# Kernel optimization log

Hardware: AMD Instinct MI355X
Metric: run time of the kernel (lower is better)

The kernel has to match this reference:

```python
import jax, jax.numpy as jnp
import numpy as np

B, S, E, H = 2, 2048, 1024, 16
DH = E // H


def setup_inputs() -> dict:
    key = jax.random.key(0)
    ks = jax.random.split(key, 9)
    inp = {
        "query": jax.random.normal(ks[0], (B, S, E), dtype=jnp.float32),
        "key": jax.random.normal(ks[1], (B, S, E), dtype=jnp.float32),
        "value": jax.random.normal(ks[2], (B, S, E), dtype=jnp.float32),
        # causal mask: True means "masked out" (masked_fill semantics)
        "mask": jnp.broadcast_to(
            jnp.triu(jnp.ones((S, S), dtype=bool), k=1)[None, None], (B, 1, S, S)
        ),
        # learned parameters (nn.Linear weight is [out, in]; y = x @ W.T + b)
        "Wq": jax.random.normal(ks[3], (E, E), dtype=jnp.float32) / np.sqrt(E),
        "Wk": jax.random.normal(ks[4], (E, E), dtype=jnp.float32) / np.sqrt(E),
        "Wv": jax.random.normal(ks[5], (E, E), dtype=jnp.float32) / np.sqrt(E),
        "Wo": jax.random.normal(ks[6], (E, E), dtype=jnp.float32) / np.sqrt(E),
        "bo": jax.random.normal(ks[7], (E,), dtype=jnp.float32) * 0.01,
    }
    return inp


def reference(query, key, value, mask, Wq, Wk, Wv, Wo, bo):
    # projections (no bias for q/k/v)
    Q = query @ Wq.T  # [B,S,E]
    K = key @ Wk.T
    V = value @ Wv.T
    # split heads: [B,S,E] -> [B,H,S,Dh]
    Q = Q.reshape(B, S, H, DH).transpose(0, 2, 1, 3)
    K = K.reshape(B, S, H, DH).transpose(0, 2, 1, 3)
    V = V.reshape(B, S, H, DH).transpose(0, 2, 1, 3)
    scale = 1.0 / np.sqrt(DH).astype(np.float32)
    scores = jnp.einsum("bhqd,bhkd->bhqk", Q, K) * scale  # [B,H,S,S]
    scores = jnp.where(mask, -jnp.inf, scores)
    attn = jax.nn.softmax(scores, axis=-1)
    # dropout(p=0.2) is identity in eval mode
    out = jnp.einsum("bhqk,bhkd->bhqd", attn, V)  # [B,H,S,Dh]
    out = out.transpose(0, 2, 1, 3).reshape(B, S, E)
    return out @ Wo.T + bo
```

## Files before the change

### kernel.cpp

```cpp
#include <hip/hip_runtime.h>
#include <hip/hip_bf16.h>
#include <stdint.h>

#define Bb 2
#define Ss 2048
#define Ee 1024
#define Hh 16
#define Dh 64

typedef __bf16 bf16_t;
typedef __attribute__((ext_vector_type(8))) __bf16 bf16x8;
typedef __attribute__((ext_vector_type(4))) __bf16 bf16x4;
typedef __attribute__((ext_vector_type(4))) float f32x4;

#define QSCALE_LOG2E 0.18033688011112042f

__device__ inline void gload_lds16(const void* g, void* l) {
  __builtin_amdgcn_global_load_lds((__attribute__((address_space(1))) void*)g,
                                   (__attribute__((address_space(3))) void*)l,
                                   16, 0, 0);
}

__device__ inline void wg_barrier() {
  asm volatile("s_barrier" ::: "memory");
}

__device__ __forceinline__ int p_addr(int q, int kv) {
  return q * 256 + ((((kv >> 3) ^ q) & 15) << 4) + (kv & 7) * 2;
}

struct Cvt7 {
  const float* s[7];
  bf16_t* d[7];
  int n8[7];
};

__global__ __launch_bounds__(256) void cvt_f32_bf16(Cvt7 c) {
  int gid = blockIdx.x * 256 + threadIdx.x;
#pragma unroll
  for (int j = 0; j < 7; ++j) {
    if (gid < c.n8[j]) {
      const float* s = c.s[j] + (size_t)gid * 8;
      const f32x4 lo = *(const f32x4*)s;
      const f32x4 hi = *(const f32x4*)(s + 4);
      bf16x8 v;
      v[0] = (bf16_t)lo[0]; v[1] = (bf16_t)lo[1];
      v[2] = (bf16_t)lo[2]; v[3] = (bf16_t)lo[3];
      v[4] = (bf16_t)hi[0]; v[5] = (bf16_t)hi[1];
      v[6] = (bf16_t)hi[2]; v[7] = (bf16_t)hi[3];
      *(bf16x8*)(c.d[j] + (size_t)gid * 8) = v;
      return;
    }
    gid -= c.n8[j];
  }
}

template <int ROWS>
__device__ __forceinline__ void stage_bf16(const bf16_t* __restrict__ src,
                                           int ldk, int k0, bf16_t* lds,
                                           int wave, int lane) {
  const int srow = lane >> 3, sslot = lane & 7;
#pragma unroll
  for (int r = 0; r < ROWS / 32; ++r) {
    const int chunk = wave + r * 4;
    const int row = chunk * 8 + srow;
    const int k16 = sslot ^ (row & 7);
    gload_lds16(src + (size_t)row * ldk + k0 + k16 * 8, lds + chunk * 512);
  }
}

template <typename EPI>
__device__ __forceinline__ void gemm_128x64(const bf16_t* Arow,
                                            const bf16_t* Wrow, bf16_t* As,
                                            bf16_t* Bs, int wave, int lane,
                                            EPI epi) {
  const int lr = lane & 15, lg = lane >> 4;
  f32x4 acc[2][4] = {};

  stage_bf16<128>(Arow, Ee, 0, As, wave, lane);
  stage_bf16<64>(Wrow, Ee, 0, Bs, wave, lane);
  stage_bf16<128>(Arow, Ee, 64, As + 8192, wave, lane);
  stage_bf16<64>(Wrow, Ee, 64, Bs + 4096, wave, lane);

  for (int t = 0; t < 16; ++t) {
    const int cur = t & 1;
    if (t < 15)
      asm volatile("s_waitcnt vmcnt(6)" ::: "memory");
    else
      asm volatile("s_waitcnt vmcnt(0)" ::: "memory");
    wg_barrier();

    const char* a_base = (const char*)(As + cur * 8192);
    const char* b_base = (const char*)(Bs + cur * 4096);
#pragma unroll
    for (int kk = 0; kk < 2; ++kk) {
      bf16x8 af[2], bfr[4];
#pragma unroll
      for (int x = 0; x < 2; ++x) {
        const int arow = wave * 32 + x * 16 + lr;
        af[x] = *(const bf16x8*)(a_base + ((arow * 128 + kk * 64 + lg * 16) ^
                                           ((arow & 7) << 4)));
      }
#pragma unroll
      for (int ni = 0; ni < 4; ++ni) {
        const int brow = ni * 16 + lr;
        bfr[ni] = *(const bf16x8*)(b_base + ((brow * 128 + kk * 64 + lg * 16) ^
                                             ((brow & 7) << 4)));
      }
#pragma unroll
      for (int mi = 0; mi < 2; ++mi)
#pragma unroll
        for (int ni = 0; ni < 4; ++ni)
          acc[mi][ni] = __builtin_amdgcn_mfma_f32_16x16x32_bf16(
              af[mi], bfr[ni], acc[mi][ni], 0, 0, 0);
    }
    wg_barrier();
    if (t + 2 < 16) {
      stage_bf16<128>(Arow, Ee, (t + 2) * 64, As + cur * 8192, wave, lane);
      stage_bf16<64>(Wrow, Ee, (t + 2) * 64, Bs + cur * 4096, wave, lane);
    }
  }

#pragma unroll
  for (int mi = 0; mi < 2; ++mi)
#pragma unroll
    for (int i = 0; i < 4; ++i) {
      const int mloc = wave * 32 + mi * 16 + lg * 4 + i;
#pragma unroll
      for (int ni = 0; ni < 4; ++ni)
        epi(mloc, ni * 16 + lr, acc[mi][ni][i]);
    }
}

__global__ __launch_bounds__(256) void qkv_proj(
    const bf16_t* __restrict__ Aq, const bf16_t* __restrict__ Ak,
    const bf16_t* __restrict__ Av, const bf16_t* __restrict__ Wq,
    const bf16_t* __restrict__ Wk, const bf16_t* __restrict__ Wv,
    bf16_t* __restrict__ Cq, bf16_t* __restrict__ Ck,
    bf16_t* __restrict__ Cv) {
  __shared__ bf16_t As[2][128 * 64];
  __shared__ bf16_t Bs[2][64 * 64];
  const int z = blockIdx.z;
  const bf16_t* A = (z == 0) ? Aq : (z == 1) ? Ak : Av;
  const bf16_t* W = (z == 0) ? Wq : (z == 1) ? Wk : Wv;
  bf16_t* C = (z == 0) ? Cq : (z == 1) ? Ck : Cv;

  const int wg = blockIdx.y * 16 + blockIdx.x;
  const int virt = (wg & 7) * 64 + (wg >> 3);
  const int n0 = (virt & 15) * 64, m0 = (virt >> 4) * 128;

  const int lane = threadIdx.x & 63, wave = threadIdx.x >> 6;

  gemm_128x64(A + (size_t)m0 * Ee, W + (size_t)n0 * Ee, As[0], Bs[0], wave,
              lane, [&](int mloc, int nloc, float v) {
                const int m = m0 + mloc, n = n0 + nloc;
                if (z == 0) v *= QSCALE_LOG2E;
                const int b = m >> 11, s = m & (Ss - 1);
                const int h = n >> 6, d = n & 63;
                if (z != 2)
                  C[(((size_t)(b * Hh + h)) * Ss + s) * Dh + d] = (bf16_t)v;
                else
                  C[(((size_t)(b * Hh + h)) * Dh + d) * Ss + s] = (bf16_t)v;
              });
}

__global__ __launch_bounds__(256) void out_gemm(const bf16_t* __restrict__ A,
                                                const bf16_t* __restrict__ W,
                                                const float* __restrict__ bias,
                                                float* __restrict__ C) {
  __shared__ bf16_t As[2][128 * 64];
  __shared__ bf16_t Bs[2][64 * 64];
  const int wg = blockIdx.y * 16 + blockIdx.x;
  const int virt = (wg & 7) * 64 + (wg >> 3);
  const int n0 = (virt & 15) * 64, m0 = (virt >> 4) * 128;

  const int lane = threadIdx.x & 63, wave = threadIdx.x >> 6;

  gemm_128x64(A + (size_t)m0 * Ee, W + (size_t)n0 * Ee, As[0], Bs[0], wave,
              lane, [&](int mloc, int nloc, float v) {
                const int n = n0 + nloc;
                C[(size_t)(m0 + mloc) * Ee + n] = v + bias[n];
              });
}


__device__ __forceinline__ void attn_stage(const bf16_t* Kh, const bf16_t* Vh,
                                           int kv0, int wave, int lane,
                                           bf16_t* KsBuf, bf16_t* VsBuf) {
#pragma unroll
  for (int r = 0; r < 4; ++r) {
    const int c = wave + r * 4;
    const int krow = c * 8 + (lane >> 3);
    const int ks = (lane & 7) ^ (krow & 7);
    gload_lds16(Kh + (size_t)(kv0 + krow) * Dh + ks * 8, KsBuf + c * 512);
    const int vrow = c * 4 + (lane >> 4);
    const int vs = (lane & 15) ^ (vrow & 7);
    gload_lds16(Vh + (size_t)vrow * Ss + kv0 + vs * 8, VsBuf + c * 512);
  }
}

template <int NI, bool MASKED>
__device__ __forceinline__ void attn_tile_compute(
    int kv0, int qw, int lane, char* pb, const char* kb, const char* vb,
    const bf16x8 aq[2], float& m_run, float& l_run, f32x4 oacc[4]) {
  const int lr = lane & 15, lg = lane >> 4;

  f32x4 sc[NI];
#pragma unroll
  for (int ni = 0; ni < NI; ++ni) {
    const int krow = ni * 16 + lr;
    const bf16x8 ak0 =
        *(const bf16x8*)(kb + ((krow * 128 + lg * 16) ^ ((krow & 7) << 4)));
    const bf16x8 ak1 = *(const bf16x8*)(kb + ((krow * 128 + 64 + lg * 16) ^
                                              ((krow & 7) << 4)));
    f32x4 z = {0.f, 0.f, 0.f, 0.f};
    z = __builtin_amdgcn_mfma_f32_16x16x32_bf16(ak0, aq[0], z, 0, 0, 0);
    z = __builtin_amdgcn_mfma_f32_16x16x32_bf16(ak1, aq[1], z, 0, 0, 0);
    sc[ni] = z;
  }

  if (MASKED) {
    const int q_rel = qw + lr - kv0;
#pragma unroll
    for (int ni = 0; ni < NI; ++ni)
#pragma unroll
      for (int i = 0; i < 4; ++i)
        if (ni * 16 + lg * 4 + i > q_rel) sc[ni][i] = -1e30f;
  }

  f32x4 vm = sc[0];
#pragma unroll
  for (int ni = 1; ni < NI; ++ni)
#pragma unroll
    for (int i = 0; i < 4; ++i) vm[i] = fmaxf(vm[i], sc[ni][i]);
  float rm = fmaxf(fmaxf(vm[0], vm[1]), fmaxf(vm[2], vm[3]));
  rm = fmaxf(rm, __shfl_xor(rm, 16));
  rm = fmaxf(rm, __shfl_xor(rm, 32));

  const float mo = m_run;
  const float mn = fmaxf(mo, rm);
  const float corr = __builtin_amdgcn_exp2f(mo - mn);
  m_run = mn;

  f32x4 vs = {0.f, 0.f, 0.f, 0.f};
#pragma unroll
  for (int ni = 0; ni < NI; ++ni) {
    bf16x4 w;
#pragma unroll
    for (int i = 0; i < 4; ++i) {
      const float p = __builtin_amdgcn_exp2f(sc[ni][i] - mn);
      vs[i] += p;
      w[i] = (bf16_t)p;
    }
    *(bf16x4*)(pb + p_addr(lr, ni * 16 + lg * 4)) = w;
  }
  float rs = (vs[0] + vs[1]) + (vs[2] + vs[3]);
  rs += __shfl_xor(rs, 16);
  rs += __shfl_xor(rs, 32);
  l_run = l_run * corr + rs;

#pragma unroll
  for (int i = 0; i < 4; ++i) {
    const float ci = __shfl(corr, (lane & 48) | (lg * 4 + i));
#pragma unroll
    for (int di = 0; di < 4; ++di) oacc[di][i] *= ci;
  }

#pragma unroll
  for (int kk = 0; kk < NI / 2; ++kk) {
    const bf16x8 pa = *(const bf16x8*)(pb + p_addr(lr, kk * 32 + lg * 8));
#pragma unroll
    for (int di = 0; di < 4; ++di) {
      const int vrow = di * 16 + lr;
      const bf16x8 bv = *(const bf16x8*)(vb + ((vrow * 256 + kk * 64 +
                                                lg * 16) ^
                                               ((vrow & 7) << 4)));
      oacc[di] =
          __builtin_amdgcn_mfma_f32_16x16x32_bf16(pa, bv, oacc[di], 0, 0, 0);
    }
  }
}

__device__ __forceinline__ void flash_qtile(int qt, const bf16_t* Qh,
                                            const bf16_t* Kh, const bf16_t* Vh,
                                            bf16_t* AO_row, int wave, int lane,
                                            bf16_t* Ks, bf16_t* Vs,
                                            bf16_t* PsW) {
  const int lr = lane & 15, lg = lane >> 4;
  const int qw = qt * 64 + wave * 16;

  bf16x8 aq[2];
#pragma unroll
  for (int kd = 0; kd < 2; ++kd)
    aq[kd] = *(const bf16x8*)(Qh + (size_t)(qw + lr) * Dh + kd * 32 + lg * 8);

  f32x4 oacc[4] = {};
  float m_run = -1e30f, l_run = 0.f;
  char* pb = (char*)PsW;

  const int nt = (qt + 2) >> 1;
  attn_stage(Kh, Vh, 0, wave, lane, Ks, Vs);

  for (int t = 0; t < nt; ++t) {
    const int cur = t & 1;
    if (t + 1 < nt) {
      attn_stage(Kh, Vh, (t + 1) * 128, wave, lane, Ks + (cur ^ 1) * 8192,
                 Vs + (cur ^ 1) * 8192);
      asm volatile("s_waitcnt vmcnt(8)" ::: "memory");
    } else {
      asm volatile("s_waitcnt vmcnt(0)" ::: "memory");
    }
    wg_barrier();
    const char* kb = (const char*)(Ks + cur * 8192);
    const char* vb = (const char*)(Vs + cur * 8192);
    if (t < nt - 1)
      attn_tile_compute<8, false>(t * 128, qw, lane, pb, kb, vb, aq, m_run,
                                  l_run, oacc);
    else if ((qt & 1) == 0)
      attn_tile_compute<4, true>(t * 128, qw, lane, pb, kb, vb, aq, m_run,
                                 l_run, oacc);
    else
      attn_tile_compute<8, true>(t * 128, qw, lane, pb, kb, vb, aq, m_run,
                                 l_run, oacc);
    wg_barrier();
  }

#pragma unroll
  for (int i = 0; i < 4; ++i) {
    const float li = __shfl(l_run, (lane & 48) | (lg * 4 + i));
    const float inv = 1.0f / li;
    const int s = qw + lg * 4 + i;
#pragma unroll
    for (int di = 0; di < 4; ++di) {
      const int d = di * 16 + lr;
      AO_row[(size_t)s * Ee + d] = (bf16_t)(oacc[di][i] * inv);
    }
  }
}

__global__ __launch_bounds__(256, 2) void attn_causal(
    const bf16_t* __restrict__ Qg, const bf16_t* __restrict__ Kg,
    const bf16_t* __restrict__ Vg, bf16_t* __restrict__ AO) {
  const int wg = blockIdx.y * 16 + blockIdx.x;
  const int virt = (wg & 7) * 64 + (wg >> 3);
  const int qx = virt & 15;
  const int bh = virt >> 4;

  const int tid = threadIdx.x;
  const int lane = tid & 63, wave = tid >> 6;

  const bf16_t* Qh = Qg + (size_t)bh * Ss * Dh;
  const bf16_t* Kh = Kg + (size_t)bh * Ss * Dh;
  const bf16_t* Vh = Vg + (size_t)bh * Dh * Ss;
  const int b = bh >> 4, h = bh & 15;
  bf16_t* AO_row = AO + (size_t)b * Ss * Ee + h * 64;

  __shared__ bf16_t Ks[2][128 * 64];
  __shared__ bf16_t Vs[2][64 * 128];
  __shared__ bf16_t Ps[4][16 * 128];

  const int qtA = qx;
  const int qtB = 31 - qx;
  flash_qtile(qtA, Qh, Kh, Vh, AO_row, wave, lane, Ks[0], Vs[0], Ps[wave]);
  flash_qtile(qtB, Qh, Kh, Vh, AO_row, wave, lane, Ks[0], Vs[0], Ps[wave]);
}

extern "C" void kernel_launch(void* const* d_in, const int* in_sizes, int n_in,
                              void* d_out, int out_size, void* d_ws,
                              size_t ws_size, hipStream_t stream) {
  const float* query = (const float*)d_in[0];
  const float* key = (const float*)d_in[1];
  const float* value = (const float*)d_in[2];
  const float* Wq = (const float*)d_in[4];
  const float* Wk = (const float*)d_in[5];
  const float* Wv = (const float*)d_in[6];
  const float* Wo = (const float*)d_in[7];
  const float* bo = (const float*)d_in[8];

  const size_t T = (size_t)Bb * Ss * Ee;
  const size_t WN = (size_t)Ee * Ee;
  bf16_t* qbf = (bf16_t*)d_ws;
  bf16_t* kbf = qbf + T;
  bf16_t* vbf = kbf + T;
  bf16_t* wqb = vbf + T;
  bf16_t* wkb = wqb + WN;
  bf16_t* wvb = wkb + WN;
  bf16_t* wob = wvb + WN;
  bf16_t* qws = wob + WN;
  bf16_t* kws = qws + T;
  bf16_t* vws = kws + T;
  bf16_t* aows = qbf;

  Cvt7 c;
  c.s[0] = query; c.d[0] = qbf; c.n8[0] = (int)(T / 8);
  c.s[1] = key;   c.d[1] = kbf; c.n8[1] = (int)(T / 8);
  c.s[2] = value; c.d[2] = vbf; c.n8[2] = (int)(T / 8);
  c.s[3] = Wq;    c.d[3] = wqb; c.n8[3] = (int)(WN / 8);
  c.s[4] = Wk;    c.d[4] = wkb; c.n8[4] = (int)(WN / 8);
  c.s[5] = Wv;    c.d[5] = wvb; c.n8[5] = (int)(WN / 8);
  c.s[6] = Wo;    c.d[6] = wob; c.n8[6] = (int)(WN / 8);
  const int total8 = (int)((3 * T + 4 * WN) / 8);

  dim3 blk(256);
  cvt_f32_bf16<<<dim3(total8 / 256), blk, 0, stream>>>(c);
  qkv_proj<<<dim3(Ee / 64, (Bb * Ss) / 128, 3), blk, 0, stream>>>(
      qbf, kbf, vbf, wqb, wkb, wvb, qws, kws, vws);
  attn_causal<<<dim3(16, Bb * Hh), blk, 0, stream>>>(qws, kws, vws, aows);
  out_gemm<<<dim3(Ee / 64, (Bb * Ss) / 128), blk, 0, stream>>>(
      aows, wob, bo, (float*)d_out);
}
```

Measured before the change: 113.3 us.

## Give each attention wave two 16-row query blocks with half the waves

The attention kernel now runs 2 waves of 128 threads per workgroup instead of 4, and each wave handles 32 query rows (two 16-row sub-tiles) instead of 16. Each K and V fragment read from LDS feeds two MFMAs, which halves LDS reads per unit of compute. Each wave now issues twice as many async global-to-LDS loads, so the waitcnt threshold is raised to match. The risks are higher register pressure and fewer waves per workgroup to hide latency, since the grid size is unchanged and total resident waves drop.

After: 124.1 us. +9.6%, slower.

```diff
diff --git a/kernel.cpp b/kernel.cpp
--- a/kernel.cpp
+++ b/kernel.cpp
@@ -188,8 +188,8 @@
                                            int kv0, int wave, int lane,
                                            bf16_t* KsBuf, bf16_t* VsBuf) {
 #pragma unroll
-  for (int r = 0; r < 4; ++r) {
-    const int c = wave + r * 4;
+  for (int r = 0; r < 8; ++r) {
+    const int c = wave + r * 2;
     const int krow = c * 8 + (lane >> 3);
     const int ks = (lane & 7) ^ (krow & 7);
     gload_lds16(Kh + (size_t)(kv0 + krow) * Dh + ks * 8, KsBuf + c * 512);
@@ -202,10 +202,10 @@
 template <int NI, bool MASKED>
 __device__ __forceinline__ void attn_tile_compute(
     int kv0, int qw, int lane, char* pb, const char* kb, const char* vb,
-    const bf16x8 aq[2], float& m_run, float& l_run, f32x4 oacc[4]) {
+    const bf16x8 aq[2][2], float m_run[2], float l_run[2], f32x4 oacc[2][4]) {
   const int lr = lane & 15, lg = lane >> 4;
 
-  f32x4 sc[NI];
+  f32x4 sc[2][NI];
 #pragma unroll
   for (int ni = 0; ni < NI; ++ni) {
     const int krow = ni * 16 + lr;
@@ -213,70 +213,83 @@
         *(const bf16x8*)(kb + ((krow * 128 + lg * 16) ^ ((krow & 7) << 4)));
     const bf16x8 ak1 = *(const bf16x8*)(kb + ((krow * 128 + 64 + lg * 16) ^
                                               ((krow & 7) << 4)));
-    f32x4 z = {0.f, 0.f, 0.f, 0.f};
-    z = __builtin_amdgcn_mfma_f32_16x16x32_bf16(ak0, aq[0], z, 0, 0, 0);
-    z = __builtin_amdgcn_mfma_f32_16x16x32_bf16(ak1, aq[1], z, 0, 0, 0);
-    sc[ni] = z;
-  }
-
-  if (MASKED) {
-    const int q_rel = qw + lr - kv0;
-#pragma unroll
-    for (int ni = 0; ni < NI; ++ni)
-#pragma unroll
-      for (int i = 0; i < 4; ++i)
-        if (ni * 16 + lg * 4 + i > q_rel) sc[ni][i] = -1e30f;
-  }
-
-  f32x4 vm = sc[0];
-#pragma unroll
-  for (int ni = 1; ni < NI; ++ni)
-#pragma unroll
-    for (int i = 0; i < 4; ++i) vm[i] = fmaxf(vm[i], sc[ni][i]);
-  float rm = fmaxf(fmaxf(vm[0], vm[1]), fmaxf(vm[2], vm[3]));
-  rm = fmaxf(rm, __shfl_xor(rm, 16));
-  rm = fmaxf(rm, __shfl_xor(rm, 32));
-
-  const float mo = m_run;
-  const float mn = fmaxf(mo, rm);
-  const float corr = __builtin_amdgcn_exp2f(mo - mn);
-  m_run = mn;
-
-  f32x4 vs = {0.f, 0.f, 0.f, 0.f};
-#pragma unroll
-  for (int ni = 0; ni < NI; ++ni) {
-    bf16x4 w;
+#pragma unroll
+    for (int qj = 0; qj < 2; ++qj) {
+      f32x4 z = {0.f, 0.f, 0.f, 0.f};
+      z = __builtin_amdgcn_mfma_f32_16x16x32_bf16(ak0, aq[qj][0], z, 0, 0, 0);
+      z = __builtin_amdgcn_mfma_f32_16x16x32_bf16(ak1, aq[qj][1], z, 0, 0, 0);
+      sc[qj][ni] = z;
+    }
+  }
+
+  float corr[2];
+#pragma unroll
+  for (int qj = 0; qj < 2; ++qj) {
+    if (MASKED) {
+      const int q_rel = qw + qj * 16 + lr - kv0;
+#pragma unroll
+      for (int ni = 0; ni < NI; ++ni)
+#pragma unroll
+        for (int i = 0; i < 4; ++i)
+          if (ni * 16 + lg * 4 + i > q_rel) sc[qj][ni][i] = -1e30f;
+    }
+
+    f32x4 vm = sc[qj][0];
+#pragma unroll
+    for (int ni = 1; ni < NI; ++ni)
+#pragma unroll
+      for (int i = 0; i < 4; ++i) vm[i] = fmaxf(vm[i], sc[qj][ni][i]);
+    float rm = fmaxf(fmaxf(vm[0], vm[1]), fmaxf(vm[2], vm[3]));
+    rm = fmaxf(rm, __shfl_xor(rm, 16));
+    rm = fmaxf(rm, __shfl_xor(rm, 32));
+
+    const float mo = m_run[qj];
+    const float mn = fmaxf(mo, rm);
+    corr[qj] = __builtin_amdgcn_exp2f(mo - mn);
+    m_run[qj] = mn;
+
+    f32x4 vs = {0.f, 0.f, 0.f, 0.f};
+#pragma unroll
+    for (int ni = 0; ni < NI; ++ni) {
+      bf16x4 w;
+#pragma unroll
+      for (int i = 0; i < 4; ++i) {
+        const float p = __builtin_amdgcn_exp2f(sc[qj][ni][i] - mn);
+        vs[i] += p;
+        w[i] = (bf16_t)p;
+      }
+      *(bf16x4*)(pb + p_addr(qj * 16 + lr, ni * 16 + lg * 4)) = w;
+    }
+    float rs = (vs[0] + vs[1]) + (vs[2] + vs[3]);
+    rs += __shfl_xor(rs, 16);
+    rs += __shfl_xor(rs, 32);
+    l_run[qj] = l_run[qj] * corr[qj] + rs;
+
 #pragma unroll
     for (int i = 0; i < 4; ++i) {
-      const float p = __builtin_amdgcn_exp2f(sc[ni][i] - mn);
-      vs[i] += p;
-      w[i] = (bf16_t)p;
-    }
-    *(bf16x4*)(pb + p_addr(lr, ni * 16 + lg * 4)) = w;
-  }
-  float rs = (vs[0] + vs[1]) + (vs[2] + vs[3]);
-  rs += __shfl_xor(rs, 16);
-  rs += __shfl_xor(rs, 32);
-  l_run = l_run * corr + rs;
-
-#pragma unroll
-  for (int i = 0; i < 4; ++i) {
-    const float ci = __shfl(corr, (lane & 48) | (lg * 4 + i));
-#pragma unroll
-    for (int di = 0; di < 4; ++di) oacc[di][i] *= ci;
+      const float ci = __shfl(corr[qj], (lane & 48) | (lg * 4 + i));
+#pragma unroll
+      for (int di = 0; di < 4; ++di) oacc[qj][di][i] *= ci;
+    }
   }
 
 #pragma unroll
   for (int kk = 0; kk < NI / 2; ++kk) {
-    const bf16x8 pa = *(const bf16x8*)(pb + p_addr(lr, kk * 32 + lg * 8));
+    bf16x8 pa[2];
+#pragma unroll
+    for (int qj = 0; qj < 2; ++qj)
+      pa[qj] =
+          *(const bf16x8*)(pb + p_addr(qj * 16 + lr, kk * 32 + lg * 8));
 #pragma unroll
     for (int di = 0; di < 4; ++di) {
       const int vrow = di * 16 + lr;
       const bf16x8 bv = *(const bf16x8*)(vb + ((vrow * 256 + kk * 64 +
                                                 lg * 16) ^
                                                ((vrow & 7) << 4)));
-      oacc[di] =
-          __builtin_amdgcn_mfma_f32_16x16x32_bf16(pa, bv, oacc[di], 0, 0, 0);
+#pragma unroll
+      for (int qj = 0; qj < 2; ++qj)
+        oacc[qj][di] = __builtin_amdgcn_mfma_f32_16x16x32_bf16(
+            pa[qj], bv, oacc[qj][di], 0, 0, 0);
     }
   }
 }
@@ -287,15 +300,18 @@
                                             bf16_t* Ks, bf16_t* Vs,
                                             bf16_t* PsW) {
   const int lr = lane & 15, lg = lane >> 4;
-  const int qw = qt * 64 + wave * 16;
-
-  bf16x8 aq[2];
-#pragma unroll
-  for (int kd = 0; kd < 2; ++kd)
-    aq[kd] = *(const bf16x8*)(Qh + (size_t)(qw + lr) * Dh + kd * 32 + lg * 8);
-
-  f32x4 oacc[4] = {};
-  float m_run = -1e30f, l_run = 0.f;
+  const int qw = qt * 64 + wave * 32;
+
+  bf16x8 aq[2][2];
+#pragma unroll
+  for (int qj = 0; qj < 2; ++qj)
+#pragma unroll
+    for (int kd = 0; kd < 2; ++kd)
+      aq[qj][kd] = *(const bf16x8*)(Qh + (size_t)(qw + qj * 16 + lr) * Dh +
+                                    kd * 32 + lg * 8);
+
+  f32x4 oacc[2][4] = {};
+  float m_run[2] = {-1e30f, -1e30f}, l_run[2] = {0.f, 0.f};
   char* pb = (char*)PsW;
 
   const int nt = (qt + 2) >> 1;
@@ -306,7 +322,7 @@
     if (t + 1 < nt) {
       attn_stage(Kh, Vh, (t + 1) * 128, wave, lane, Ks + (cur ^ 1) * 8192,
                  Vs + (cur ^ 1) * 8192);
-      asm volatile("s_waitcnt vmcnt(8)" ::: "memory");
+      asm volatile("s_waitcnt vmcnt(16)" ::: "memory");
     } else {
       asm volatile("s_waitcnt vmcnt(0)" ::: "memory");
     }
@@ -326,19 +342,22 @@
   }
 
 #pragma unroll
-  for (int i = 0; i < 4; ++i) {
-    const float li = __shfl(l_run, (lane & 48) | (lg * 4 + i));
-    const float inv = 1.0f / li;
-    const int s = qw + lg * 4 + i;
-#pragma unroll
-    for (int di = 0; di < 4; ++di) {
-      const int d = di * 16 + lr;
-      AO_row[(size_t)s * Ee + d] = (bf16_t)(oacc[di][i] * inv);
-    }
-  }
-}
-
-__global__ __launch_bounds__(256, 2) void attn_causal(
+  for (int qj = 0; qj < 2; ++qj) {
+#pragma unroll
+    for (int i = 0; i < 4; ++i) {
+      const float li = __shfl(l_run[qj], (lane & 48) | (lg * 4 + i));
+      const float inv = 1.0f / li;
+      const int s = qw + qj * 16 + lg * 4 + i;
+#pragma unroll
+      for (int di = 0; di < 4; ++di) {
+        const int d = di * 16 + lr;
+        AO_row[(size_t)s * Ee + d] = (bf16_t)(oacc[qj][di][i] * inv);
+      }
+    }
+  }
+}
+
+__global__ __launch_bounds__(128, 2) void attn_causal(
     const bf16_t* __restrict__ Qg, const bf16_t* __restrict__ Kg,
     const bf16_t* __restrict__ Vg, bf16_t* __restrict__ AO) {
   const int wg = blockIdx.y * 16 + blockIdx.x;
@@ -357,7 +376,7 @@
 
   __shared__ bf16_t Ks[2][128 * 64];
   __shared__ bf16_t Vs[2][64 * 128];
-  __shared__ bf16_t Ps[4][16 * 128];
+  __shared__ bf16_t Ps[2][32 * 128];
 
   const int qtA = qx;
   const int qtB = 31 - qx;
@@ -405,7 +424,8 @@
   cvt_f32_bf16<<<dim3(total8 / 256), blk, 0, stream>>>(c);
   qkv_proj<<<dim3(Ee / 64, (Bb * Ss) / 128, 3), blk, 0, stream>>>(
       qbf, kbf, vbf, wqb, wkb, wvb, qws, kws, vws);
-  attn_causal<<<dim3(16, Bb * Hh), blk, 0, stream>>>(qws, kws, vws, aows);
+  attn_causal<<<dim3(16, Bb * Hh), dim3(128), 0, stream>>>(qws, kws, vws,
+                                                           aows);
   out_gemm<<<dim3(Ee / 64, (Bb * Ss) / 128), blk, 0, stream>>>(
       aows, wob, bo, (float*)d_out);
 }
```

## Fuse paired causal q-tiles into one KV sweep sharing staged K/V tiles

Applied to the files above, without the earlier changes.

Instead of processing the two paired query tiles (qx and 31-qx) sequentially, each reloading K/V from tile 0, the kernel now walks the KV sequence once for the longer tile and also computes the shorter tile while its range is active. This removes the duplicated K/V global loads and LDS staging for the shorter tile. In exchange it keeps two sets of accumulators and Q fragments live, which raises register pressure and could affect occupancy at launch_bounds(256,2). It also adds an unused run_tile helper.

Result: no change. 113.9 us (+0.6%).

```diff
diff --git a/kernel.cpp b/kernel.cpp
--- a/kernel.cpp
+++ b/kernel.cpp
@@ -281,61 +281,14 @@
   }
 }
 
-__device__ __forceinline__ void flash_qtile(int qt, const bf16_t* Qh,
-                                            const bf16_t* Kh, const bf16_t* Vh,
-                                            bf16_t* AO_row, int wave, int lane,
-                                            bf16_t* Ks, bf16_t* Vs,
-                                            bf16_t* PsW) {
-  const int lr = lane & 15, lg = lane >> 4;
-  const int qw = qt * 64 + wave * 16;
-
-  bf16x8 aq[2];
-#pragma unroll
-  for (int kd = 0; kd < 2; ++kd)
-    aq[kd] = *(const bf16x8*)(Qh + (size_t)(qw + lr) * Dh + kd * 32 + lg * 8);
-
-  f32x4 oacc[4] = {};
-  float m_run = -1e30f, l_run = 0.f;
-  char* pb = (char*)PsW;
-
-  const int nt = (qt + 2) >> 1;
-  attn_stage(Kh, Vh, 0, wave, lane, Ks, Vs);
-
-  for (int t = 0; t < nt; ++t) {
-    const int cur = t & 1;
-    if (t + 1 < nt) {
-      attn_stage(Kh, Vh, (t + 1) * 128, wave, lane, Ks + (cur ^ 1) * 8192,
-                 Vs + (cur ^ 1) * 8192);
-      asm volatile("s_waitcnt vmcnt(8)" ::: "memory");
-    } else {
-      asm volatile("s_waitcnt vmcnt(0)" ::: "memory");
-    }
-    wg_barrier();
-    const char* kb = (const char*)(Ks + cur * 8192);
-    const char* vb = (const char*)(Vs + cur * 8192);
-    if (t < nt - 1)
-      attn_tile_compute<8, false>(t * 128, qw, lane, pb, kb, vb, aq, m_run,
-                                  l_run, oacc);
-    else if ((qt & 1) == 0)
-      attn_tile_compute<4, true>(t * 128, qw, lane, pb, kb, vb, aq, m_run,
-                                 l_run, oacc);
-    else
-      attn_tile_compute<8, true>(t * 128, qw, lane, pb, kb, vb, aq, m_run,
-                                 l_run, oacc);
-    wg_barrier();
-  }
-
-#pragma unroll
-  for (int i = 0; i < 4; ++i) {
-    const float li = __shfl(l_run, (lane & 48) | (lg * 4 + i));
-    const float inv = 1.0f / li;
-    const int s = qw + lg * 4 + i;
-#pragma unroll
-    for (int di = 0; di < 4; ++di) {
-      const int d = di * 16 + lr;
-      AO_row[(size_t)s * Ee + d] = (bf16_t)(oacc[di][i] * inv);
-    }
-  }
+template <typename F>
+__device__ __forceinline__ void run_tile(int t, int nt, int qt, F f) {
+  if (t < nt - 1)
+    f(std::integral_constant<int, 8>{}, std::integral_constant<bool, false>{});
+  else if ((qt & 1) == 0)
+    f(std::integral_constant<int, 4>{}, std::integral_constant<bool, true>{});
+  else
+    f(std::integral_constant<int, 8>{}, std::integral_constant<bool, true>{});
 }
 
 __global__ __launch_bounds__(256, 2) void attn_causal(
@@ -348,6 +301,7 @@
 
   const int tid = threadIdx.x;
   const int lane = tid & 63, wave = tid >> 6;
+  const int lr = lane & 15, lg = lane >> 4;
 
   const bf16_t* Qh = Qg + (size_t)bh * Ss * Dh;
   const bf16_t* Kh = Kg + (size_t)bh * Ss * Dh;
@@ -361,8 +315,77 @@
 
   const int qtA = qx;
   const int qtB = 31 - qx;
-  flash_qtile(qtA, Qh, Kh, Vh, AO_row, wave, lane, Ks[0], Vs[0], Ps[wave]);
-  flash_qtile(qtB, Qh, Kh, Vh, AO_row, wave, lane, Ks[0], Vs[0], Ps[wave]);
+  const int qwA = qtA * 64 + wave * 16;
+  const int qwB = qtB * 64 + wave * 16;
+
+  bf16x8 aqA[2], aqB[2];
+#pragma unroll
+  for (int kd = 0; kd < 2; ++kd) {
+    aqA[kd] =
+        *(const bf16x8*)(Qh + (size_t)(qwA + lr) * Dh + kd * 32 + lg * 8);
+    aqB[kd] =
+        *(const bf16x8*)(Qh + (size_t)(qwB + lr) * Dh + kd * 32 + lg * 8);
+  }
+
+  f32x4 oaccA[4] = {}, oaccB[4] = {};
+  float mA = -1e30f, lA = 0.f, mB = -1e30f, lB = 0.f;
+  char* pb = (char*)Ps[wave];
+
+  const int ntA = (qtA + 2) >> 1;
+  const int ntB = (qtB + 2) >> 1;
+
+  attn_stage(Kh, Vh, 0, wave, lane, Ks[0], Vs[0]);
+
+  for (int t = 0; t < ntB; ++t) {
+    const int cur = t & 1;
+    if (t + 1 < ntB) {
+      attn_stage(Kh, Vh, (t + 1) * 128, wave, lane, Ks[cur ^ 1], Vs[cur ^ 1]);
+      asm volatile("s_waitcnt vmcnt(8)" ::: "memory");
+    } else {
+      asm volatile("s_waitcnt vmcnt(0)" ::: "memory");
+    }
+    wg_barrier();
+    const char* kb = (const char*)Ks[cur];
+    const char* vb = (const char*)Vs[cur];
+
+    if (t < ntA) {
+      if (t < ntA - 1)
+        attn_tile_compute<8, false>(t * 128, qwA, lane, pb, kb, vb, aqA, mA,
+                                    lA, oaccA);
+      else if ((qtA & 1) == 0)
+        attn_tile_compute<4, true>(t * 128, qwA, lane, pb, kb, vb, aqA, mA,
+                                   lA, oaccA);
+      else
+        attn_tile_compute<8, true>(t * 128, qwA, lane, pb, kb, vb, aqA, mA,
+                                   lA, oaccA);
+    }
+    if (t < ntB - 1)
+      attn_tile_compute<8, false>(t * 128, qwB, lane, pb, kb, vb, aqB, mB, lB,
+                                  oaccB);
+    else if ((qtB & 1) == 0)
+      attn_tile_compute<4, true>(t * 128, qwB, lane, pb, kb, vb, aqB, mB, lB,
+                                 oaccB);
+    else
+      attn_tile_compute<8, true>(t * 128, qwB, lane, pb, kb, vb, aqB, mB, lB,
+                                 oaccB);
+    wg_barrier();
+  }
+
+#pragma unroll
+  for (int i = 0; i < 4; ++i) {
+    const float liA = __shfl(lA, (lane & 48) | (lg * 4 + i));
+    const float invA = 1.0f / liA;
+    const int sA = qwA + lg * 4 + i;
+    const float liB = __shfl(lB, (lane & 48) | (lg * 4 + i));
+    const float invB = 1.0f / liB;
+    const int sB = qwB + lg * 4 + i;
+#pragma unroll
+    for (int di = 0; di < 4; ++di) {
+      const int d = di * 16 + lr;
+      AO_row[(size_t)sA * Ee + d] = (bf16_t)(oaccA[di][i] * invA);
+      AO_row[(size_t)sB * Ee + d] = (bf16_t)(oaccB[di][i] * invB);
+    }
+  }
 }
 
 extern "C" void kernel_launch(void* const* d_in, const int* in_sizes, int n_in,
```

## Fuse fp32-to-bf16 activation conversion into QKV projection GEMM

Applied to the files above, without the earlier changes.

The separate conversion of query/key/value activations to bf16 is removed, and the QKV projection now loads fp32 activations into registers, converts them, and writes swizzled bf16 into shared memory. The weight-only conversion kernel remains. This avoids writing and re-reading three bf16 activation tensors, but each GEMM tile now reads fp32 A from global memory (16 times across the N tiles), holds more registers for the prefetch, and uses a single A buffer with extra barriers.

Result: slower. 128.6 us (+13.5%).

```diff
diff --git a/kernel.cpp b/kernel.cpp
--- a/kernel.cpp
+++ b/kernel.cpp
@@ -29,16 +29,16 @@
   return q * 256 + ((((kv >> 3) ^ q) & 15) << 4) + (kv & 7) * 2;
 }
 
-struct Cvt7 {
-  const float* s[7];
-  bf16_t* d[7];
-  int n8[7];
+struct Cvt4 {
+  const float* s[4];
+  bf16_t* d[4];
+  int n8[4];
 };
 
-__global__ __launch_bounds__(256) void cvt_f32_bf16(Cvt7 c) {
+__global__ __launch_bounds__(256) void cvt_f32_bf16(Cvt4 c) {
   int gid = blockIdx.x * 256 + threadIdx.x;
 #pragma unroll
-  for (int j = 0; j < 7; ++j) {
+  for (int j = 0; j < 4; ++j) {
     if (gid < c.n8[j]) {
       const float* s = c.s[j] + (size_t)gid * 8;
       const f32x4 lo = *(const f32x4*)s;
@@ -133,15 +133,15 @@
 }
 
 __global__ __launch_bounds__(256) void qkv_proj(
-    const bf16_t* __restrict__ Aq, const bf16_t* __restrict__ Ak,
-    const bf16_t* __restrict__ Av, const bf16_t* __restrict__ Wq,
+    const float* __restrict__ Aq, const float* __restrict__ Ak,
+    const float* __restrict__ Av, const bf16_t* __restrict__ Wq,
     const bf16_t* __restrict__ Wk, const bf16_t* __restrict__ Wv,
     bf16_t* __restrict__ Cq, bf16_t* __restrict__ Ck,
     bf16_t* __restrict__ Cv) {
-  __shared__ bf16_t As[2][128 * 64];
+  __shared__ bf16_t As[128 * 64];
   __shared__ bf16_t Bs[2][64 * 64];
   const int z = blockIdx.z;
-  const bf16_t* A = (z == 0) ? Aq : (z == 1) ? Ak : Av;
+  const float* A = (z == 0) ? Aq : (z == 1) ? Ak : Av;
   const bf16_t* W = (z == 0) ? Wq : (z == 1) ? Wk : Wv;
   bf16_t* C = (z == 0) ? Cq : (z == 1) ? Ck : Cv;
 
@@ -149,19 +149,125 @@
   const int virt = (wg & 7) * 64 + (wg >> 3);
   const int n0 = (virt & 15) * 64, m0 = (virt >> 4) * 128;
 
-  const int lane = threadIdx.x & 63, wave = threadIdx.x >> 6;
-
-  gemm_128x64(A + (size_t)m0 * Ee, W + (size_t)n0 * Ee, As[0], Bs[0], wave,
-              lane, [&](int mloc, int nloc, float v) {
-                const int m = m0 + mloc, n = n0 + nloc;
-                if (z == 0) v *= QSCALE_LOG2E;
-                const int b = m >> 11, s = m & (Ss - 1);
-                const int h = n >> 6, d = n & 63;
-                if (z != 2)
-                  C[(((size_t)(b * Hh + h)) * Ss + s) * Dh + d] = (bf16_t)v;
-                else
-                  C[(((size_t)(b * Hh + h)) * Dh + d) * Ss + s] = (bf16_t)v;
-              });
+  const int tid = threadIdx.x;
+  const int lane = tid & 63, wave = tid >> 6;
+  const int lr = lane & 15, lg = lane >> 4;
+  const int srow = lane >> 3, sslot = lane & 7;
+
+  const float* Arow = A + (size_t)m0 * Ee;
+  const bf16_t* Wrow = W + (size_t)n0 * Ee;
+
+  int rowv[4], wadr[4];
+#pragma unroll
+  for (int r = 0; r < 4; ++r) {
+    rowv[r] = (wave + r * 4) * 8 + srow;
+    wadr[r] = (rowv[r] * 128 + sslot * 16) ^ ((rowv[r] & 7) << 4);
+  }
+
+  f32x4 acc[2][4] = {};
+  f32x4 rA[4][2], rB[4][2];
+
+  auto loadA = [&](int t, f32x4(&ra)[4][2]) {
+#pragma unroll
+    for (int r = 0; r < 4; ++r) {
+      const float* s = Arow + (size_t)rowv[r] * Ee + t * 64 + sslot * 8;
+      ra[r][0] = *(const f32x4*)s;
+      ra[r][1] = *(const f32x4*)(s + 4);
+    }
+  };
+  auto writeA = [&](f32x4(&ra)[4][2]) {
+#pragma unroll
+    for (int r = 0; r < 4; ++r) {
+      bf16x8 v;
+#pragma unroll
+      for (int i = 0; i < 4; ++i) {
+        v[i] = (bf16_t)ra[r][0][i];
+        v[4 + i] = (bf16_t)ra[r][1][i];
+      }
+      *(bf16x8*)((char*)As + wadr[r]) = v;
+    }
+  };
+  auto compute = [&](const bf16_t* bsbuf) {
+    const char* a_base = (const char*)As;
+    const char* b_base = (const char*)bsbuf;
+#pragma unroll
+    for (int kk = 0; kk < 2; ++kk) {
+      bf16x8 af[2], bfr[4];
+#pragma unroll
+      for (int x = 0; x < 2; ++x) {
+        const int arow = wave * 32 + x * 16 + lr;
+        af[x] = *(const bf16x8*)(a_base + ((arow * 128 + kk * 64 + lg * 16) ^
+                                           ((arow & 7) << 4)));
+      }
+#pragma unroll
+      for (int ni = 0; ni < 4; ++ni) {
+        const int brow = ni * 16 + lr;
+        bfr[ni] = *(const bf16x8*)(b_base + ((brow * 128 + kk * 64 + lg * 16) ^
+                                             ((brow & 7) << 4)));
+      }
+#pragma unroll
+      for (int mi = 0; mi < 2; ++mi)
+#pragma unroll
+        for (int ni = 0; ni < 4; ++ni)
+          acc[mi][ni] = __builtin_amdgcn_mfma_f32_16x16x32_bf16(
+              af[mi], bfr[ni], acc[mi][ni], 0, 0, 0);
+    }
+  };
+
+  loadA(0, rA);
+  stage_bf16<64>(Wrow, Ee, 0, Bs[0], wave, lane);
+  loadA(1, rB);
+  stage_bf16<64>(Wrow, Ee, 64, Bs[1], wave, lane);
+
+  for (int tt = 0; tt < 8; ++tt) {
+    const int t0 = 2 * tt, t1 = t0 + 1;
+    if (t0 < 15)
+      asm volatile("s_waitcnt vmcnt(10)" ::: "memory");
+    else
+      asm volatile("s_waitcnt vmcnt(0)" ::: "memory");
+    writeA(rA);
+    asm volatile("s_waitcnt lgkmcnt(0)" ::: "memory");
+    wg_barrier();
+    compute(Bs[0]);
+    wg_barrier();
+    if (t0 + 2 < 16) {
+      loadA(t0 + 2, rA);
+      stage_bf16<64>(Wrow, Ee, (t0 + 2) * 64, Bs[0], wave, lane);
+    }
+    if (t1 < 15)
+      asm volatile("s_waitcnt vmcnt(10)" ::: "memory");
+    else
+      asm volatile("s_waitcnt vmcnt(0)" ::: "memory");
+    writeA(rB);
+    asm volatile("s_waitcnt lgkmcnt(0)" ::: "memory");
+    wg_barrier();
+    compute(Bs[1]);
+    wg_barrier();
+    if (t1 + 2 < 16) {
+      loadA(t1 + 2, rB);
+      stage_bf16<64>(Wrow, Ee, (t1 + 2) * 64, Bs[1], wave, lane);
+    }
+  }
+
+#pragma unroll
+  for (int mi = 0; mi < 2; ++mi) {
+#pragma unroll
+    for (int i = 0; i < 4; ++i) {
+      const int m = m0 + wave * 32 + mi * 16 + lg * 4 + i;
+#pragma unroll
+      for (int ni = 0; ni < 4; ++ni) {
+        const int n = n0 + ni * 16 + lr;
+        float v = acc[mi][ni][i];
+        if (z == 0) v *= QSCALE_LOG2E;
+        const int b = m >> 11, s = m & (Ss - 1);
+        const int h = n >> 6, d = n & 63;
+        if (z != 2)
+          C[(((size_t)(b * Hh + h)) * Ss + s) * Dh + d] = (bf16_t)v;
+        else
+          C[(((size_t)(b * Hh + h)) * Dh + d) * Ss + s] = (bf16_t)v;
+      }
+    }
+  }
 }
 
 __global__ __launch_bounds__(256) void out_gemm(const bf16_t* __restrict__ A,
@@ -182,7 +288,6 @@
                 C[(size_t)(m0 + mloc) * Ee + n] = v + bias[n];
               });
 }
-
 
 __device__ __forceinline__ void attn_stage(const bf16_t* Kh, const bf16_t* Vh,
                                            int kv0, int wave, int lane,
@@ -379,32 +484,26 @@
 
   const size_t T = (size_t)Bb * Ss * Ee;
   const size_t WN = (size_t)Ee * Ee;
-  bf16_t* qbf = (bf16_t*)d_ws;
-  bf16_t* kbf = qbf + T;
-  bf16_t* vbf = kbf + T;
-  bf16_t* wqb = vbf + T;
+  bf16_t* wqb = (bf16_t*)d_ws;
   bf16_t* wkb = wqb + WN;
   bf16_t* wvb = wkb + WN;
   bf16_t* wob = wvb + WN;
   bf16_t* qws = wob + WN;
   bf16_t* kws = qws + T;
   bf16_t* vws = kws + T;
-  bf16_t* aows = qbf;
-
-  Cvt7 c;
-  c.s[0] = query; c.d[0] = qbf; c.n8[0] = (int)(T / 8);
-  c.s[1] = key;   c.d[1] = kbf; c.n8[1] = (int)(T / 8);
-  c.s[2] = value; c.d[2] = vbf; c.n8[2] = (int)(T / 8);
-  c.s[3] = Wq;    c.d[3] = wqb; c.n8[3] = (int)(WN / 8);
-  c.s[4] = Wk;    c.d[4] = wkb; c.n8[4] = (int)(WN / 8);
-  c.s[5] = Wv;    c.d[5] = wvb; c.n8[5] = (int)(WN / 8);
-  c.s[6] = Wo;    c.d[6] = wob; c.n8[6] = (int)(WN / 8);
-  const int total8 = (int)((3 * T + 4 * WN) / 8);
+  bf16_t* aows = vws + T;
+
+  Cvt4 c;
+  c.s[0] = Wq; c.d[0] = wqb; c.n8[0] = (int)(WN / 8);
+  c.s[1] = Wk; c.d[1] = wkb; c.n8[1] = (int)(WN / 8);
+  c.s[2] = Wv; c.d[2] = wvb; c.n8[2] = (int)(WN / 8);
+  c.s[3] = Wo; c.d[3] = wob; c.n8[3] = (int)(WN / 8);
+  const int total8 = (int)((4 * WN) / 8);
 
   dim3 blk(256);
   cvt_f32_bf16<<<dim3(total8 / 256), blk, 0, stream>>>(c);
   qkv_proj<<<dim3(Ee / 64, (Bb * Ss) / 128, 3), blk, 0, stream>>>(
-      qbf, kbf, vbf, wqb, wkb, wvb, qws, kws, vws);
+      query, key, value, wqb, wkb, wvb, qws, kws, vws);
   attn_causal<<<dim3(16, Bb * Hh), blk, 0, stream>>>(qws, kws, vws, aows);
   out_gemm<<<dim3(Ee / 64, (Bb * Ss) / 128), blk, 0, stream>>>(
       aows, wob, bo, (float*)d_out);
```
